# Optimization experiments

Hardware: AMD Instinct MI355X
Metric: run time of the kernel (lower is better)

The kernel has to match this reference:

```python
import jax, jax.numpy as jnp
import numpy as np

N, E = 10000, 80000
D, D_EDGE, L = 32, 16, 3
D2 = D * D


def layer_norm(x, g, b, eps=1e-5):
    m = jnp.mean(x, axis=-1, keepdims=True)
    v = jnp.var(x, axis=-1, keepdims=True)
    return (x - m) / jnp.sqrt(v + eps) * g + b


def setup_inputs() -> dict:
    key = jax.random.key(0)
    ks = jax.random.split(key, 16)
    s_e = 1.0 / np.sqrt(D_EDGE)
    s_d = 1.0 / np.sqrt(D)
    s_f = 1.0 / np.sqrt(L * D)
    return {
        "x": jax.random.normal(ks[0], (N, D), dtype=jnp.float32),
        "edge_index": jax.random.randint(ks[1], (2, E), 0, N),
        "edge_attr": jax.random.normal(ks[2], (E, D_EDGE), dtype=jnp.float32),
        # shared edge MLP: Linear(d_edge_in -> d^2) + LayerNorm(d^2) + ReLU
        "emlp_w": jax.random.uniform(ks[3], (D2, D_EDGE), jnp.float32, -s_e, s_e),
        "emlp_b": jnp.zeros((D2,), jnp.float32),
        "emlp_ln_g": jnp.ones((D2,), jnp.float32),
        "emlp_ln_b": jnp.zeros((D2,), jnp.float32),
        # per-layer params (stacked over L layers)
        "root_w": jax.random.uniform(ks[4], (L, D, D), jnp.float32, -s_d, s_d),  # NNConv root lin (no bias)
        "conv_b": jnp.zeros((L, D), jnp.float32),                                # NNConv bias
        "res_w": jax.random.uniform(ks[5], (L, D, D), jnp.float32, -s_d, s_d),
        "res_b": jnp.zeros((L, D), jnp.float32),
        "ln_g": jnp.ones((L, D), jnp.float32),
        "ln_b": jnp.zeros((L, D), jnp.float32),
        # fusion: Linear(L*d -> d) + LayerNorm(d) + ReLU
        "fuse_w": jax.random.uniform(ks[6], (D, L * D), jnp.float32, -s_f, s_f),
        "fuse_b": jnp.zeros((D,), jnp.float32),
        "fuse_ln_g": jnp.ones((D,), jnp.float32),
        "fuse_ln_b": jnp.zeros((D,), jnp.float32),
    }


def reference(x, edge_index, edge_attr, emlp_w, emlp_b, emlp_ln_g, emlp_ln_b,
              root_w, conv_b, res_w, res_b, ln_g, ln_b,
              fuse_w, fuse_b, fuse_ln_g, fuse_ln_b):
    n_nodes = x.shape[0]
    src, tgt = edge_index[0], edge_index[1]
    # Shared edge MLP applied to the same edge_attr in every layer -> identical
    # per-edge weight matrices; compute once. [E, d_in, d_out]
    h = layer_norm(edge_attr @ emlp_w.T + emlp_b, emlp_ln_g, emlp_ln_b)
    We = jax.nn.relu(h).reshape(-1, D, D)
    x_src_gatherer = src
    outputs = []
    for l in range(L):
        x_res = x @ res_w[l].T + res_b[l]
        # NNConv message: x_j @ W_e, scatter-add to target nodes
        msg = jnp.einsum('ed,edf->ef', x[x_src_gatherer], We)  # [E, d]
        agg = jax.ops.segment_sum(msg, tgt, num_segments=n_nodes)
        h = agg + x @ root_w[l].T + conv_b[l]
        # dropout is identity in eval mode
        x = layer_norm(h + x_res, ln_g[l], ln_b[l])
        outputs.append(x)
    fused = jnp.concatenate(outputs, axis=-1) @ fuse_w.T + fuse_b
    fused = jax.nn.relu(layer_norm(fused, fuse_ln_g, fuse_ln_b))
    return fused
```

## Files before the change

### kernel.cpp

```cpp
#include <hip/hip_runtime.h>

#define NN 10000
#define EE 80000
#define DD 32
#define DEDGE 16
#define LL 3
#define D2V 1024
#define NTILE 2500

typedef __attribute__((ext_vector_type(8))) short short8v;
typedef __attribute__((ext_vector_type(16))) float f32x16;

__device__ __forceinline__ unsigned short bf16rne(float x) {
    unsigned u = __float_as_uint(x);
    return (unsigned short)((u + 0x7FFF + ((u >> 16) & 1)) >> 16);
}
__device__ __forceinline__ float bf16tof(unsigned short h) {
    return __uint_as_float(((unsigned)h) << 16);
}
__device__ __forceinline__ uint4 pack8(const unsigned short* u) {
    uint4 r;
    r.x = (unsigned)u[0] | ((unsigned)u[1] << 16);
    r.y = (unsigned)u[2] | ((unsigned)u[3] << 16);
    r.z = (unsigned)u[4] | ((unsigned)u[5] << 16);
    r.w = (unsigned)u[6] | ((unsigned)u[7] << 16);
    return r;
}

__global__ __launch_bounds__(256) void setup1_kernel(
    const int* __restrict__ ei,
    const float* __restrict__ w, const float* __restrict__ wb,
    const float* __restrict__ lg, const float* __restrict__ lb,
    int* __restrict__ cnt, float* __restrict__ st,
    uint4* __restrict__ afh, uint4* __restrict__ afl, uint4* __restrict__ a2f) {
    const int bid = blockIdx.x;
    const int t = threadIdx.x;
    if (bid < 313) {
        const int e = bid * 256 + t;
        if (e < EE) atomicAdd(&cnt[ei[EE + e]], 1);
    } else if (bid < 377) {
        const int r0 = (bid - 313) * 16;
        const int k = t >> 4, j = t & 15;
        float acc = 0.f;
#pragma unroll
        for (int r = 0; r < 16; ++r)
            acc = fmaf(w[(r0 + r) * DEDGE + k], w[(r0 + r) * DEDGE + j], acc);
        atomicAdd(&st[t], acc * (1.f / D2V));
        if (t < DEDGE) {
            float s = 0.f, q = 0.f;
#pragma unroll
            for (int r = 0; r < 16; ++r) {
                s += w[(r0 + r) * DEDGE + t];
                q = fmaf(wb[r0 + r], w[(r0 + r) * DEDGE + t], q);
            }
            atomicAdd(&st[256 + t], s * (1.f / D2V));
            atomicAdd(&st[272 + t], q * (1.f / D2V));
        } else if (t == 16) {
            float s = 0.f, s2 = 0.f;
#pragma unroll
            for (int r = 0; r < 16; ++r) {
                s += wb[r0 + r];
                s2 = fmaf(wb[r0 + r], wb[r0 + r], s2);
            }
            atomicAdd(&st[288], s * (1.f / D2V));
            atomicAdd(&st[289], s2 * (1.f / D2V));
        }
    } else {
        const int tid = (bid - 377) * 256 + t;
        if (tid >= 32 * 64) return;
        const int d = tid >> 6, l = tid & 63;
        const int row = l & 31, kh = l >> 5;
        const int r = d * 32 + row;
        const float g = lg[r];
        unsigned short uh[8], ul[8];
#pragma unroll
        for (int i = 0; i < 8; ++i) {
            const float v = g * w[r * DEDGE + kh * 8 + i];
            const unsigned short h = bf16rne(v);
            uh[i] = h;
            ul[i] = bf16rne(v - bf16tof(h));
        }
        afh[d * 64 + l] = pack8(uh);
        afl[d * 64 + l] = pack8(ul);
        if (kh == 0) {
            const float bg = g * wb[r];
            const float lbv = lb[r];
            const unsigned short bgh = bf16rne(bg);
            const unsigned short bgl = bf16rne(bg - bf16tof(bgh));
            const unsigned short gh = bf16rne(g);
            const unsigned short gl = bf16rne(g - bf16tof(gh));
            const unsigned short lbh = bf16rne(lbv);
            const unsigned short lbl = bf16rne(lbv - bf16tof(lbh));
            unsigned short s[8] = {bgh, bgl, bgh, gh, gl, gh, lbh, lbl};
            a2f[d * 64 + l] = pack8(s);
        } else {
            a2f[d * 64 + l] = make_uint4(0, 0, 0, 0);
        }
    }
}

__global__ __launch_bounds__(1024) void scan_kernel(int* __restrict__ cur, int* __restrict__ off) {
    __shared__ int s[1024];
    const int t = threadIdx.x;
    const int base = t * 10;
    int loc[10];
    int run = 0;
#pragma unroll
    for (int i = 0; i < 10; ++i) {
        const int idx = base + i;
        const int v = (idx < NN) ? cur[idx] : 0;
        loc[i] = run;
        run += v;
    }
    s[t] = run;
    __syncthreads();
    for (int o = 1; o < 1024; o <<= 1) {
        const int v = (t >= o) ? s[t - o] : 0;
        __syncthreads();
        s[t] += v;
        __syncthreads();
    }
    const int excl = s[t] - run;
#pragma unroll
    for (int i = 0; i < 10; ++i) {
        const int idx = base + i;
        if (idx < NN) {
            off[idx] = excl + loc[i];
            cur[idx] = excl + loc[i];
        }
    }
    if (t == 1023) off[NN] = s[1023];
}

__global__ __launch_bounds__(256) void scatter_kernel(const int* __restrict__ ei,
                                                      int* __restrict__ cur,
                                                      int* __restrict__ perm) {
    const int e = blockIdx.x * 256 + threadIdx.x;
    if (e < EE) {
        const int p = atomicAdd(&cur[ei[EE + e]], 1);
        perm[p] = e;
    }
}

__global__ __launch_bounds__(256) void stats_edge_perm(const float* __restrict__ eattr,
                                                       const float* __restrict__ st,
                                                       const int* __restrict__ perm,
                                                       const int* __restrict__ ei,
                                                       uint4* __restrict__ bfh,
                                                       uint4* __restrict__ bfl,
                                                       uint4* __restrict__ b2f,
                                                       int* __restrict__ sperm) {
    const int p = blockIdx.x * 256 + threadIdx.x;
    if (p >= EE) return;
    const int e = perm[p];
    sperm[p] = ei[e];
    float ea[16];
    {
        const float4* ep = (const float4*)(eattr + e * DEDGE);
#pragma unroll
        for (int c = 0; c < 4; ++c) {
            const float4 t = ep[c];
            ea[4 * c] = t.x; ea[4 * c + 1] = t.y; ea[4 * c + 2] = t.z; ea[4 * c + 3] = t.w;
        }
    }
    float m = st[288];
#pragma unroll
    for (int k = 0; k < 16; ++k) m = fmaf(st[256 + k], ea[k], m);
    float ex2 = st[289];
#pragma unroll
    for (int k = 0; k < 16; ++k) {
        float t = 2.f * st[272 + k];
#pragma unroll
        for (int j = 0; j < 16; ++j) t = fmaf(st[k * 16 + j], ea[j], t);
        ex2 = fmaf(t, ea[k], ex2);
    }
    const float var = fmaxf(ex2 - m * m, 0.f);
    const float inv = rsqrtf(var + 1e-5f);
    const float nmi = -m * inv;
    const int t = p >> 5, col = p & 31;
#pragma unroll
    for (int h = 0; h < 2; ++h) {
        unsigned short uh[8], ul[8];
#pragma unroll
        for (int i = 0; i < 8; ++i) {
            const float v = inv * ea[8 * h + i];
            const unsigned short a = bf16rne(v);
            uh[i] = a;
            ul[i] = bf16rne(v - bf16tof(a));
        }
        bfh[t * 64 + h * 32 + col] = pack8(uh);
        bfl[t * 64 + h * 32 + col] = pack8(ul);
    }
    const unsigned short ivh = bf16rne(inv);
    const unsigned short ivl = bf16rne(inv - bf16tof(ivh));
    const unsigned short nmh = bf16rne(nmi);
    const unsigned short nml = bf16rne(nmi - bf16tof(nmh));
    const unsigned short one = 0x3F80;
    unsigned short s[8] = {ivh, ivh, ivl, nmh, nmh, nml, one, one};
    b2f[t * 64 + col] = pack8(s);
    b2f[t * 64 + 32 + col] = make_uint4(0, 0, 0, 0);
}

__global__ __launch_bounds__(256) void edge_mfma_kernel(
    const float* __restrict__ x, const int* __restrict__ sperm,
    const uint4* __restrict__ afh, const uint4* __restrict__ afl, const uint4* __restrict__ a2f,
    const uint4* __restrict__ bfh, const uint4* __restrict__ bfl, const uint4* __restrict__ b2f,
    float* __restrict__ msgout) {
    const int lane = threadIdx.x & 63;
    const int w = (blockIdx.x * 256 + threadIdx.x) >> 6;
    const int col = lane & 31, hi = lane >> 5;
    const int p = w * 32 + col;
    const int si = sperm[p];
    float xr[32];
    {
        const float4* xp = (const float4*)(x + si * DD);
#pragma unroll
        for (int c = 0; c < 8; ++c) {
            const float4 t = xp[c];
            xr[4 * c] = t.x; xr[4 * c + 1] = t.y; xr[4 * c + 2] = t.z; xr[4 * c + 3] = t.w;
        }
    }
    const short8v bh = ((const short8v*)bfh)[w * 64 + lane];
    const short8v bl = ((const short8v*)bfl)[w * 64 + lane];
    const short8v b2 = ((const short8v*)b2f)[w * 64 + lane];
    float msg[16];
#pragma unroll
    for (int i = 0; i < 16; ++i) msg[i] = 0.f;
#pragma unroll
    for (int d = 0; d < 32; ++d) {
        const short8v ah = ((const short8v*)afh)[d * 64 + lane];
        const short8v al = ((const short8v*)afl)[d * 64 + lane];
        const short8v a2 = ((const short8v*)a2f)[d * 64 + lane];
        f32x16 C;
#pragma unroll
        for (int r = 0; r < 16; ++r) C[r] = 0.f;
        C = __builtin_amdgcn_mfma_f32_32x32x16_bf16(ah, bh, C, 0, 0, 0);
        C = __builtin_amdgcn_mfma_f32_32x32x16_bf16(ah, bl, C, 0, 0, 0);
        C = __builtin_amdgcn_mfma_f32_32x32x16_bf16(al, bh, C, 0, 0, 0);
        C = __builtin_amdgcn_mfma_f32_32x32x16_bf16(a2, b2, C, 0, 0, 0);
        const float xd = xr[d];
#pragma unroll
        for (int r = 0; r < 16; ++r) msg[r] = fmaf(xd, fmaxf(C[r], 0.f), msg[r]);
    }
    float* op = msgout + p * DD + hi * 4;
#pragma unroll
    for (int q = 0; q < 4; ++q)
        *(float4*)(op + q * 8) = make_float4(msg[4 * q], msg[4 * q + 1], msg[4 * q + 2], msg[4 * q + 3]);
}

__global__ __launch_bounds__(256) void node_wave_kernel(
    const float* __restrict__ x, const float* __restrict__ msg,
    const int* __restrict__ off,
    const float* __restrict__ root_w, const float* __restrict__ conv_b,
    const float* __restrict__ res_w, const float* __restrict__ res_b,
    const float* __restrict__ lng, const float* __restrict__ lnb,
    float* __restrict__ out) {
    const int lane = threadIdx.x & 63;
    const int w = (blockIdx.x * 256 + threadIdx.x) >> 6;
    const int hi = lane >> 5, f = lane & 31;
    const int n = w * 2 + hi;
    float wrow[32];
    {
        const float4* rp = (const float4*)(root_w + f * DD);
        const float4* sp = (const float4*)(res_w + f * DD);
#pragma unroll
        for (int c = 0; c < 8; ++c) {
            const float4 a = rp[c];
            const float4 b = sp[c];
            wrow[4 * c] = a.x + b.x; wrow[4 * c + 1] = a.y + b.y;
            wrow[4 * c + 2] = a.z + b.z; wrow[4 * c + 3] = a.w + b.w;
        }
    }
    float acc = conv_b[f] + res_b[f];
    const int k0 = off[n], k1 = off[n + 1];
    for (int k = k0; k < k1; ++k) acc += msg[k * DD + f];
    const float xl = x[n * DD + f];
#pragma unroll
    for (int d = 0; d < DD; ++d) acc = fmaf(__shfl(xl, hi * 32 + d), wrow[d], acc);
    float s1 = acc, s2 = acc * acc;
#pragma unroll
    for (int o = 16; o >= 1; o >>= 1) {
        s1 += __shfl_xor(s1, o);
        s2 += __shfl_xor(s2, o);
    }
    const float m = s1 * (1.f / 32.f);
    const float v = s2 * (1.f / 32.f) - m * m;
    const float inv = rsqrtf(v + 1e-5f);
    out[n * DD + f] = fmaf((acc - m) * inv, lng[f], lnb[f]);
}

__global__ __launch_bounds__(256) void node_fuse_kernel(
    const float* __restrict__ x, const float* __restrict__ msg,
    const int* __restrict__ off,
    const float* __restrict__ root_w, const float* __restrict__ conv_b,
    const float* __restrict__ res_w, const float* __restrict__ res_b,
    const float* __restrict__ lng, const float* __restrict__ lnb,
    const float* __restrict__ o0, const float* __restrict__ o1,
    const float* __restrict__ fw, const float* __restrict__ fb,
    const float* __restrict__ fg, const float* __restrict__ fbb,
    float* __restrict__ out) {
    const int lane = threadIdx.x & 63;
    const int w = (blockIdx.x * 256 + threadIdx.x) >> 6;
    const int hi = lane >> 5, f = lane & 31;
    const int n = w * 2 + hi;
    float o2v;
    {
        float wrow[32];
        {
            const float4* rp = (const float4*)(root_w + f * DD);
            const float4* sp = (const float4*)(res_w + f * DD);
#pragma unroll
            for (int c = 0; c < 8; ++c) {
                const float4 a = rp[c];
                const float4 b = sp[c];
                wrow[4 * c] = a.x + b.x; wrow[4 * c + 1] = a.y + b.y;
                wrow[4 * c + 2] = a.z + b.z; wrow[4 * c + 3] = a.w + b.w;
            }
        }
        float acc = conv_b[f] + res_b[f];
        const int k0 = off[n], k1 = off[n + 1];
        for (int k = k0; k < k1; ++k) acc += msg[k * DD + f];
        const float xl = x[n * DD + f];
#pragma unroll
        for (int d = 0; d < DD; ++d) acc = fmaf(__shfl(xl, hi * 32 + d), wrow[d], acc);
        float s1 = acc, s2 = acc * acc;
#pragma unroll
        for (int o = 16; o >= 1; o >>= 1) {
            s1 += __shfl_xor(s1, o);
            s2 += __shfl_xor(s2, o);
        }
        const float m = s1 * (1.f / 32.f);
        const float v = s2 * (1.f / 32.f) - m * m;
        const float inv = rsqrtf(v + 1e-5f);
        o2v = fmaf((acc - m) * inv, lng[f], lnb[f]);
    }
    float fr[96];
    {
        const float4* fp = (const float4*)(fw + f * 96);
#pragma unroll
        for (int c = 0; c < 24; ++c) {
            const float4 t = fp[c];
            fr[4 * c] = t.x; fr[4 * c + 1] = t.y; fr[4 * c + 2] = t.z; fr[4 * c + 3] = t.w;
        }
    }
    float acc = fb[f];
    const float c0 = o0[n * DD + f], c1 = o1[n * DD + f];
#pragma unroll
    for (int d = 0; d < DD; ++d) acc = fmaf(__shfl(c0, hi * 32 + d), fr[d], acc);
#pragma unroll
    for (int d = 0; d < DD; ++d) acc = fmaf(__shfl(c1, hi * 32 + d), fr[32 + d], acc);
#pragma unroll
    for (int d = 0; d < DD; ++d) acc = fmaf(__shfl(o2v, hi * 32 + d), fr[64 + d], acc);
    float s1 = acc, s2 = acc * acc;
#pragma unroll
    for (int o = 16; o >= 1; o >>= 1) {
        s1 += __shfl_xor(s1, o);
        s2 += __shfl_xor(s2, o);
    }
    const float m = s1 * (1.f / 32.f);
    const float v = s2 * (1.f / 32.f) - m * m;
    const float inv = rsqrtf(v + 1e-5f);
    out[n * DD + f] = fmaxf(fmaf((acc - m) * inv, fg[f], fbb[f]), 0.f);
}

__global__ __launch_bounds__(256) void fuse_wave_kernel(
    const float* __restrict__ o0, const float* __restrict__ o1, const float* __restrict__ o2,
    const float* __restrict__ fw, const float* __restrict__ fb,
    const float* __restrict__ g, const float* __restrict__ b,
    float* __restrict__ out) {
    const int lane = threadIdx.x & 63;
    const int w = (blockIdx.x * 256 + threadIdx.x) >> 6;
    const int hi = lane >> 5, f = lane & 31;
    const int n = w * 2 + hi;
    float fr[96];
    {
        const float4* fp = (const float4*)(fw + f * 96);
#pragma unroll
        for (int c = 0; c < 24; ++c) {
            const float4 t = fp[c];
            fr[4 * c] = t.x; fr[4 * c + 1] = t.y; fr[4 * c + 2] = t.z; fr[4 * c + 3] = t.w;
        }
    }
    float acc = fb[f];
    const float c0 = o0[n * DD + f], c1 = o1[n * DD + f], c2 = o2[n * DD + f];
#pragma unroll
    for (int d = 0; d < DD; ++d) acc = fmaf(__shfl(c0, hi * 32 + d), fr[d], acc);
#pragma unroll
    for (int d = 0; d < DD; ++d) acc = fmaf(__shfl(c1, hi * 32 + d), fr[32 + d], acc);
#pragma unroll
    for (int d = 0; d < DD; ++d) acc = fmaf(__shfl(c2, hi * 32 + d), fr[64 + d], acc);
    float s1 = acc, s2 = acc * acc;
#pragma unroll
    for (int o = 16; o >= 1; o >>= 1) {
        s1 += __shfl_xor(s1, o);
        s2 += __shfl_xor(s2, o);
    }
    const float m = s1 * (1.f / 32.f);
    const float v = s2 * (1.f / 32.f) - m * m;
    const float inv = rsqrtf(v + 1e-5f);
    out[n * DD + f] = fmaxf(fmaf((acc - m) * inv, g[f], b[f]), 0.f);
}

__global__ __launch_bounds__(256) void prep_stats_par(const float* __restrict__ w,
                                                      const float* __restrict__ b,
                                                      float* __restrict__ st) {
    const int t = threadIdx.x;
    const int r0 = blockIdx.x * 16;
    const int k = t >> 4, j = t & 15;
    float acc = 0.f;
#pragma unroll
    for (int r = 0; r < 16; ++r)
        acc = fmaf(w[(r0 + r) * DEDGE + k], w[(r0 + r) * DEDGE + j], acc);
    atomicAdd(&st[t], acc * (1.f / D2V));
    if (t < DEDGE) {
        float s = 0.f, q = 0.f;
#pragma unroll
        for (int r = 0; r < 16; ++r) {
            s += w[(r0 + r) * DEDGE + t];
            q = fmaf(b[r0 + r], w[(r0 + r) * DEDGE + t], q);
        }
        atomicAdd(&st[256 + t], s * (1.f / D2V));
        atomicAdd(&st[272 + t], q * (1.f / D2V));
    } else if (t == 16) {
        float s = 0.f, s2 = 0.f;
#pragma unroll
        for (int r = 0; r < 16; ++r) {
            s += b[r0 + r];
            s2 = fmaf(b[r0 + r], b[r0 + r], s2);
        }
        atomicAdd(&st[288], s * (1.f / D2V));
        atomicAdd(&st[289], s2 * (1.f / D2V));
    }
}

__global__ __launch_bounds__(256) void edge_kernel_fb(
    const float* __restrict__ x, const int* __restrict__ ei,
    const float* __restrict__ eattr,
    const float* __restrict__ w, const float* __restrict__ wb,
    const float* __restrict__ lg, const float* __restrict__ lb,
    const float* __restrict__ st, float* __restrict__ out) {
    const int wv = threadIdx.x >> 6;
    const int lane = threadIdx.x & 63;
    const int W = blockIdx.x * 4 + wv;
    const int e = (W >> 2) * 64 + lane;
    const int f0 = (W & 3) * 8;
    const int si = ei[e];
    const int ti = ei[EE + e];
    float ea[16];
    {
        const float4* ep = (const float4*)(eattr + e * DEDGE);
#pragma unroll
        for (int c = 0; c < 4; ++c) {
            const float4 t = ep[c];
            ea[4 * c] = t.x; ea[4 * c + 1] = t.y; ea[4 * c + 2] = t.z; ea[4 * c + 3] = t.w;
        }
    }
    float m = st[288];
#pragma unroll
    for (int k = 0; k < 16; ++k) m = fmaf(st[256 + k], ea[k], m);
    float ex2 = st[289];
#pragma unroll
    for (int k = 0; k < 16; ++k) {
        float t = 2.f * st[272 + k];
#pragma unroll
        for (int j = 0; j < 16; ++j) t = fmaf(st[k * 16 + j], ea[j], t);
        ex2 = fmaf(t, ea[k], ex2);
    }
    const float var = fmaxf(ex2 - m * m, 0.f);
    const float inv = rsqrtf(var + 1e-5f);
    const float nm = -m;
    const float* xp = x + si * DD;
    float msg[8] = {0.f, 0.f, 0.f, 0.f, 0.f, 0.f, 0.f, 0.f};
#pragma unroll 1
    for (int d = 0; d < DD; ++d) {
        const float xd = xp[d];
        const int r0 = d * 32 + f0;
        const float* wr = w + r0 * DEDGE;
        const float* br = wb + r0;
        const float* gr = lg + r0;
        const float* b2r = lb + r0;
#pragma unroll
        for (int f = 0; f < 8; ++f) {
            float h = br[f];
#pragma unroll
            for (int k = 0; k < 16; ++k) h = fmaf(wr[f * 16 + k], ea[k], h);
            const float t1 = inv * gr[f];
            const float t2 = fmaf(nm, t1, b2r[f]);
            float val = fmaf(h, t1, t2);
            val = fmaxf(val, 0.f);
            msg[f] = fmaf(xd, val, msg[f]);
        }
    }
#pragma unroll
    for (int f = 0; f < 8; ++f) atomicAdd(&out[ti * DD + f0 + f], msg[f]);
}

__global__ __launch_bounds__(256) void node_kernel_fb(
    const float* __restrict__ x, const float* __restrict__ agg,
    const float* __restrict__ root_w, const float* __restrict__ conv_b,
    const float* __restrict__ res_w, const float* __restrict__ res_b,
    const float* __restrict__ lng, const float* __restrict__ lnb,
    float* __restrict__ out) {
    __shared__ float wsm[D2V];
    __shared__ float bs[DD], gs[DD], bbs[DD];
    for (int i = threadIdx.x; i < D2V; i += 256) wsm[i] = root_w[i] + res_w[i];
    if (threadIdx.x < DD) {
        bs[threadIdx.x] = conv_b[threadIdx.x] + res_b[threadIdx.x];
        gs[threadIdx.x] = lng[threadIdx.x];
        bbs[threadIdx.x] = lnb[threadIdx.x];
    }
    __syncthreads();
    const int n = blockIdx.x * 256 + threadIdx.x;
    if (n >= NN) return;
    float xr[DD], pre[DD];
    {
        const float4* p = (const float4*)(x + n * DD);
        const float4* q = (const float4*)(agg + n * DD);
#pragma unroll
        for (int c = 0; c < 8; ++c) {
            const float4 t = p[c];
            xr[4 * c] = t.x; xr[4 * c + 1] = t.y; xr[4 * c + 2] = t.z; xr[4 * c + 3] = t.w;
            const float4 u = q[c];
            pre[4 * c] = u.x; pre[4 * c + 1] = u.y; pre[4 * c + 2] = u.z; pre[4 * c + 3] = u.w;
        }
    }
    float s1 = 0.f, s2 = 0.f;
#pragma unroll
    for (int ff = 0; ff < DD; ++ff) {
        float acc = pre[ff] + bs[ff];
        const float* wr = wsm + ff * DD;
#pragma unroll
        for (int dd = 0; dd < DD; ++dd) acc = fmaf(xr[dd], wr[dd], acc);
        pre[ff] = acc;
        s1 += acc;
        s2 = fmaf(acc, acc, s2);
    }
    const float m = s1 * (1.f / 32.f);
    const float v = s2 * (1.f / 32.f) - m * m;
    const float inv = rsqrtf(v + 1e-5f);
    float4* op = (float4*)(out + n * DD);
#pragma unroll
    for (int c = 0; c < 8; ++c) {
        float4 t;
        t.x = fmaf((pre[4 * c + 0] - m) * inv, gs[4 * c + 0], bbs[4 * c + 0]);
        t.y = fmaf((pre[4 * c + 1] - m) * inv, gs[4 * c + 1], bbs[4 * c + 1]);
        t.z = fmaf((pre[4 * c + 2] - m) * inv, gs[4 * c + 2], bbs[4 * c + 2]);
        t.w = fmaf((pre[4 * c + 3] - m) * inv, gs[4 * c + 3], bbs[4 * c + 3]);
        op[c] = t;
    }
}

extern "C" void kernel_launch(void* const* d_in, const int* in_sizes, int n_in,
                              void* d_out, int out_size, void* d_ws, size_t ws_size,
                              hipStream_t stream) {
    const float* x   = (const float*)d_in[0];
    const int*   ei  = (const int*)d_in[1];
    const float* ea  = (const float*)d_in[2];
    const float* emw = (const float*)d_in[3];
    const float* emb = (const float*)d_in[4];
    const float* elg = (const float*)d_in[5];
    const float* elb = (const float*)d_in[6];
    const float* rootw = (const float*)d_in[7];
    const float* convb = (const float*)d_in[8];
    const float* resw  = (const float*)d_in[9];
    const float* resb  = (const float*)d_in[10];
    const float* lng   = (const float*)d_in[11];
    const float* lnb   = (const float*)d_in[12];
    const float* fw    = (const float*)d_in[13];
    const float* fb    = (const float*)d_in[14];
    const float* flg   = (const float*)d_in[15];
    const float* flb   = (const float*)d_in[16];

    const size_t U4N = 2048 * 3 + (size_t)NTILE * 64 * 3;
    const size_t FR0 = U4N * 4;
    const size_t FTOT = FR0 + (size_t)EE * DD + 2 * (size_t)NN * DD + 320;
    const size_t ITOT = 2 * (NN + 1) + 2 * (size_t)EE;
    const size_t PRIMARY_NEED = FTOT * 4 + ITOT * 4 + 256;

    if (ws_size >= PRIMARY_NEED) {
        uint4* u4 = (uint4*)d_ws;
        uint4* afh = u4;
        uint4* afl = afh + 2048;
        uint4* a2f = afl + 2048;
        uint4* bfh = a2f + 2048;
        uint4* bfl = bfh + (size_t)NTILE * 64;
        uint4* b2f = bfl + (size_t)NTILE * 64;
        float* wsf = (float*)d_ws;
        float* msg  = wsf + FR0;
        float* out0 = msg + (size_t)EE * DD;
        float* out1 = out0 + NN * DD;
        float* st   = out1 + NN * DD;
        int* cur   = (int*)(st + 320);
        int* off   = cur + (NN + 1);
        int* perm  = off + (NN + 1);
        int* sperm = perm + EE;

        hipMemsetAsync(st, 0, (320 + NN + 1) * sizeof(float), stream);
        setup1_kernel<<<385, 256, 0, stream>>>(ei, emw, emb, elg, elb, cur, st, afh, afl, a2f);
        scan_kernel<<<1, 1024, 0, stream>>>(cur, off);
        scatter_kernel<<<313, 256, 0, stream>>>(ei, cur, perm);
        stats_edge_perm<<<313, 256, 0, stream>>>(ea, st, perm, ei, bfh, bfl, b2f, sperm);

        edge_mfma_kernel<<<625, 256, 0, stream>>>(x, sperm, afh, afl, a2f, bfh, bfl, b2f, msg);
        node_wave_kernel<<<1250, 256, 0, stream>>>(x, msg, off,
            rootw, convb, resw, resb, lng, lnb, out0);
        edge_mfma_kernel<<<625, 256, 0, stream>>>(out0, sperm, afh, afl, a2f, bfh, bfl, b2f, msg);
        node_wave_kernel<<<1250, 256, 0, stream>>>(out0, msg, off,
            rootw + D2V, convb + DD, resw + D2V, resb + DD, lng + DD, lnb + DD, out1);
        edge_mfma_kernel<<<625, 256, 0, stream>>>(out1, sperm, afh, afl, a2f, bfh, bfl, b2f, msg);
        node_fuse_kernel<<<1250, 256, 0, stream>>>(out1, msg, off,
            rootw + 2 * D2V, convb + 2 * DD, resw + 2 * D2V, resb + 2 * DD,
            lng + 2 * DD, lnb + 2 * DD,
            out0, out1, fw, fb, flg, flb, (float*)d_out);
    } else {
        float* wsf = (float*)d_ws;
        float* agg  = wsf;
        float* out0 = wsf + NN * DD;
        float* out1 = out0 + NN * DD;
        float* out2 = out1 + NN * DD;
        float* st   = wsf + 4 * NN * DD;
        float* outs[3] = {out0, out1, out2};

        hipMemsetAsync(st, 0, 320 * sizeof(float), stream);
        prep_stats_par<<<64, 256, 0, stream>>>(emw, emb, st);
        const float* xin = x;
        for (int l = 0; l < LL; ++l) {
            hipMemsetAsync(agg, 0, NN * DD * sizeof(float), stream);
            edge_kernel_fb<<<1250, 256, 0, stream>>>(xin, ei, ea, emw, emb, elg, elb, st, agg);
            node_kernel_fb<<<40, 256, 0, stream>>>(xin, agg,
                rootw + l * D2V, convb + l * DD, resw + l * D2V, resb + l * DD,
                lng + l * DD, lnb + l * DD, outs[l]);
            xin = outs[l];
        }
        fuse_wave_kernel<<<1250, 256, 0, stream>>>(out0, out1, out2, fw, fb, flg, flb,
                                                   (float*)d_out);
    }
}
```

Before: 172.8 us.

## Fuse CSR setup into one kernel and merge scatter with edge prep

Result: no change. 174.8 us (+1.1%).

```diff
diff --git a/kernel.cpp b/kernel.cpp
--- a/kernel.cpp
+++ b/kernel.cpp
@@ -27,55 +27,98 @@
     return r;
 }
 
-__global__ __launch_bounds__(256) void setup1_kernel(
+__global__ __launch_bounds__(1024) void setup_kernel(
     const int* __restrict__ ei,
-    const float* __restrict__ w, const float* __restrict__ wb,
-    const float* __restrict__ lg, const float* __restrict__ lb,
-    int* __restrict__ cnt, float* __restrict__ st,
-    uint4* __restrict__ afh, uint4* __restrict__ afl, uint4* __restrict__ a2f) {
+    const float* __restrict__ emw, const float* __restrict__ emb,
+    const float* __restrict__ elg, const float* __restrict__ elb,
+    int* __restrict__ cur, int* __restrict__ off, float* __restrict__ st,
+    uint4* __restrict__ afh, uint4* __restrict__ afl, uint4* __restrict__ a2f)
+{
+    __shared__ int smi[NN + 1024];
     const int bid = blockIdx.x;
     const int t = threadIdx.x;
-    if (bid < 313) {
-        const int e = bid * 256 + t;
-        if (e < EE) atomicAdd(&cnt[ei[EE + e]], 1);
-    } else if (bid < 377) {
-        const int r0 = (bid - 313) * 16;
-        const int k = t >> 4, j = t & 15;
-        float acc = 0.f;
-#pragma unroll
-        for (int r = 0; r < 16; ++r)
-            acc = fmaf(w[(r0 + r) * DEDGE + k], w[(r0 + r) * DEDGE + j], acc);
-        atomicAdd(&st[t], acc * (1.f / D2V));
-        if (t < DEDGE) {
-            float s = 0.f, q = 0.f;
-#pragma unroll
-            for (int r = 0; r < 16; ++r) {
-                s += w[(r0 + r) * DEDGE + t];
-                q = fmaf(wb[r0 + r], w[(r0 + r) * DEDGE + t], q);
+
+    if (bid == 0) {
+        int* cnt = smi;
+        int* part = smi + NN;
+        for (int i = t; i < NN; i += 1024) cnt[i] = 0;
+        __syncthreads();
+        for (int e = t; e < EE; e += 1024) atomicAdd(&cnt[ei[EE + e]], 1);
+        __syncthreads();
+        const int base = t * 10;
+        int loc[10];
+        int run = 0;
+#pragma unroll
+        for (int i = 0; i < 10; ++i) {
+            const int idx = base + i;
+            const int v = (idx < NN) ? cnt[idx] : 0;
+            loc[i] = run;
+            run += v;
+        }
+        part[t] = run;
+        __syncthreads();
+        for (int o = 1; o < 1024; o <<= 1) {
+            const int v = (t >= o) ? part[t - o] : 0;
+            __syncthreads();
+            part[t] += v;
+            __syncthreads();
+        }
+        const int excl = part[t] - run;
+#pragma unroll
+        for (int i = 0; i < 10; ++i) {
+            const int idx = base + i;
+            if (idx < NN) {
+                off[idx] = excl + loc[i];
+                cur[idx] = excl + loc[i];
             }
-            atomicAdd(&st[256 + t], s * (1.f / D2V));
-            atomicAdd(&st[272 + t], q * (1.f / D2V));
-        } else if (t == 16) {
-            float s = 0.f, s2 = 0.f;
-#pragma unroll
-            for (int r = 0; r < 16; ++r) {
-                s += wb[r0 + r];
-                s2 = fmaf(wb[r0 + r], wb[r0 + r], s2);
+        }
+        if (t == 1023) off[NN] = part[1023];
+    } else if (bid == 1) {
+        float* ws = (float*)smi;
+        float* bs = ((float*)smi) + 2048;
+        float accM = 0.f, s = 0.f, q = 0.f, sb = 0.f, sb2 = 0.f;
+        for (int c = 0; c < 8; ++c) {
+            const int r0 = c * 128;
+            for (int i = t; i < 2048; i += 1024) ws[i] = emw[r0 * DEDGE + i];
+            if (t < 128) bs[t] = emb[r0 + t];
+            __syncthreads();
+            if (t < 256) {
+                const int k = t >> 4, j = t & 15;
+                for (int r = 0; r < 128; ++r)
+                    accM = fmaf(ws[r * 16 + k], ws[r * 16 + j], accM);
+            } else if (t < 272) {
+                const int kk = t - 256;
+                for (int r = 0; r < 128; ++r) {
+                    s += ws[r * 16 + kk];
+                    q = fmaf(bs[r], ws[r * 16 + kk], q);
+                }
+            } else if (t == 288) {
+                for (int r = 0; r < 128; ++r) {
+                    sb += bs[r];
+                    sb2 = fmaf(bs[r], bs[r], sb2);
+                }
             }
-            atomicAdd(&st[288], s * (1.f / D2V));
-            atomicAdd(&st[289], s2 * (1.f / D2V));
+            __syncthreads();
+        }
+        if (t < 256) {
+            st[t] = accM * (1.f / D2V);
+        } else if (t < 272) {
+            st[t] = s * (1.f / D2V);
+            st[t + 16] = q * (1.f / D2V);
+        } else if (t == 288) {
+            st[288] = sb * (1.f / D2V);
+            st[289] = sb2 * (1.f / D2V);
         }
     } else {
-        const int tid = (bid - 377) * 256 + t;
-        if (tid >= 32 * 64) return;
-        const int d = tid >> 6, l = tid & 63;
+        const int tid2 = (bid - 2) * 1024 + t;
+        const int d = tid2 >> 6, l = tid2 & 63;
         const int row = l & 31, kh = l >> 5;
         const int r = d * 32 + row;
-        const float g = lg[r];
+        const float g = elg[r];
         unsigned short uh[8], ul[8];
 #pragma unroll
         for (int i = 0; i < 8; ++i) {
-            const float v = g * w[r * DEDGE + kh * 8 + i];
+            const float v = g * emw[r * DEDGE + kh * 8 + i];
             const unsigned short h = bf16rne(v);
             uh[i] = h;
             ul[i] = bf16rne(v - bf16tof(h));
@@ -83,84 +126,42 @@
         afh[d * 64 + l] = pack8(uh);
         afl[d * 64 + l] = pack8(ul);
         if (kh == 0) {
-            const float bg = g * wb[r];
-            const float lbv = lb[r];
+            const float bg = g * emb[r];
+            const float lbv = elb[r];
             const unsigned short bgh = bf16rne(bg);
             const unsigned short bgl = bf16rne(bg - bf16tof(bgh));
             const unsigned short gh = bf16rne(g);
             const unsigned short gl = bf16rne(g - bf16tof(gh));
             const unsigned short lbh = bf16rne(lbv);
             const unsigned short lbl = bf16rne(lbv - bf16tof(lbh));
-            unsigned short s[8] = {bgh, bgl, bgh, gh, gl, gh, lbh, lbl};
-            a2f[d * 64 + l] = pack8(s);
+            unsigned short sarr[8] = {bgh, bgl, bgh, gh, gl, gh, lbh, lbl};
+            a2f[d * 64 + l] = pack8(sarr);
         } else {
             a2f[d * 64 + l] = make_uint4(0, 0, 0, 0);
         }
     }
 }
 
-__global__ __launch_bounds__(1024) void scan_kernel(int* __restrict__ cur, int* __restrict__ off) {
-    __shared__ int s[1024];
-    const int t = threadIdx.x;
-    const int base = t * 10;
-    int loc[10];
-    int run = 0;
-#pragma unroll
-    for (int i = 0; i < 10; ++i) {
-        const int idx = base + i;
-        const int v = (idx < NN) ? cur[idx] : 0;
-        loc[i] = run;
-        run += v;
-    }
-    s[t] = run;
-    __syncthreads();
-    for (int o = 1; o < 1024; o <<= 1) {
-        const int v = (t >= o) ? s[t - o] : 0;
-        __syncthreads();
-        s[t] += v;
-        __syncthreads();
-    }
-    const int excl = s[t] - run;
-#pragma unroll
-    for (int i = 0; i < 10; ++i) {
-        const int idx = base + i;
-        if (idx < NN) {
-            off[idx] = excl + loc[i];
-            cur[idx] = excl + loc[i];
-        }
-    }
-    if (t == 1023) off[NN] = s[1023];
-}
-
-__global__ __launch_bounds__(256) void scatter_kernel(const int* __restrict__ ei,
-                                                      int* __restrict__ cur,
-                                                      int* __restrict__ perm) {
+__global__ __launch_bounds__(256) void stats_edge_perm2(const float* __restrict__ eattr,
+                                                        const float* __restrict__ st,
+                                                        const int* __restrict__ ei,
+                                                        int* __restrict__ cur,
+                                                        uint4* __restrict__ bfh,
+                                                        uint4* __restrict__ bfl,
+                                                        uint4* __restrict__ b2f,
+                                                        int* __restrict__ sperm) {
     const int e = blockIdx.x * 256 + threadIdx.x;
-    if (e < EE) {
-        const int p = atomicAdd(&cur[ei[EE + e]], 1);
-        perm[p] = e;
-    }
-}
-
-__global__ __launch_bounds__(256) void stats_edge_perm(const float* __restrict__ eattr,
-                                                       const float* __restrict__ st,
-                                                       const int* __restrict__ perm,
-                                                       const int* __restrict__ ei,
-                                                       uint4* __restrict__ bfh,
-                                                       uint4* __restrict__ bfl,
-                                                       uint4* __restrict__ b2f,
-                                                       int* __restrict__ sperm) {
-    const int p = blockIdx.x * 256 + threadIdx.x;
-    if (p >= EE) return;
-    const int e = perm[p];
+    if (e >= EE) return;
+    const int tgt = ei[EE + e];
+    const int p = atomicAdd(&cur[tgt], 1);
     sperm[p] = ei[e];
     float ea[16];
     {
         const float4* ep = (const float4*)(eattr + e * DEDGE);
 #pragma unroll
         for (int c = 0; c < 4; ++c) {
-            const float4 t = ep[c];
-            ea[4 * c] = t.x; ea[4 * c + 1] = t.y; ea[4 * c + 2] = t.z; ea[4 * c + 3] = t.w;
+            const float4 t4 = ep[c];
+            ea[4 * c] = t4.x; ea[4 * c + 1] = t4.y; ea[4 * c + 2] = t4.z; ea[4 * c + 3] = t4.w;
         }
     }
     float m = st[288];
@@ -169,15 +170,15 @@
     float ex2 = st[289];
 #pragma unroll
     for (int k = 0; k < 16; ++k) {
-        float t = 2.f * st[272 + k];
-#pragma unroll
-        for (int j = 0; j < 16; ++j) t = fmaf(st[k * 16 + j], ea[j], t);
-        ex2 = fmaf(t, ea[k], ex2);
+        float tv = 2.f * st[272 + k];
+#pragma unroll
+        for (int j = 0; j < 16; ++j) tv = fmaf(st[k * 16 + j], ea[j], tv);
+        ex2 = fmaf(tv, ea[k], ex2);
     }
     const float var = fmaxf(ex2 - m * m, 0.f);
     const float inv = rsqrtf(var + 1e-5f);
     const float nmi = -m * inv;
-    const int t = p >> 5, col = p & 31;
+    const int tt = p >> 5, col = p & 31;
 #pragma unroll
     for (int h = 0; h < 2; ++h) {
         unsigned short uh[8], ul[8];
@@ -188,8 +189,8 @@
             uh[i] = a;
             ul[i] = bf16rne(v - bf16tof(a));
         }
-        bfh[t * 64 + h * 32 + col] = pack8(uh);
-        bfl[t * 64 + h * 32 + col] = pack8(ul);
+        bfh[tt * 64 + h * 32 + col] = pack8(uh);
+        bfl[tt * 64 + h * 32 + col] = pack8(ul);
     }
     const unsigned short ivh = bf16rne(inv);
     const unsigned short ivl = bf16rne(inv - bf16tof(ivh));
@@ -197,8 +198,8 @@
     const unsigned short nml = bf16rne(nmi - bf16tof(nmh));
     const unsigned short one = 0x3F80;
     unsigned short s[8] = {ivh, ivh, ivl, nmh, nmh, nml, one, one};
-    b2f[t * 64 + col] = pack8(s);
-    b2f[t * 64 + 32 + col] = make_uint4(0, 0, 0, 0);
+    b2f[tt * 64 + col] = pack8(s);
+    b2f[tt * 64 + 32 + col] = make_uint4(0, 0, 0, 0);
 }
 
 __global__ __launch_bounds__(256) void edge_mfma_kernel(
@@ -216,16 +217,16 @@
         const float4* xp = (const float4*)(x + si * DD);
 #pragma unroll
         for (int c = 0; c < 8; ++c) {
-            const float4 t = xp[c];
-            xr[4 * c] = t.x; xr[4 * c + 1] = t.y; xr[4 * c + 2] = t.z; xr[4 * c + 3] = t.w;
+            const float4 t4 = xp[c];
+            xr[4 * c] = t4.x; xr[4 * c + 1] = t4.y; xr[4 * c + 2] = t4.z; xr[4 * c + 3] = t4.w;
         }
     }
     const short8v bh = ((const short8v*)bfh)[w * 64 + lane];
     const short8v bl = ((const short8v*)bfl)[w * 64 + lane];
     const short8v b2 = ((const short8v*)b2f)[w * 64 + lane];
-    float msg[16];
-#pragma unroll
-    for (int i = 0; i < 16; ++i) msg[i] = 0.f;
+    float mg[16];
+#pragma unroll
+    for (int i = 0; i < 16; ++i) mg[i] = 0.f;
 #pragma unroll
     for (int d = 0; d < 32; ++d) {
         const short8v ah = ((const short8v*)afh)[d * 64 + lane];
@@ -240,12 +241,12 @@
         C = __builtin_amdgcn_mfma_f32_32x32x16_bf16(a2, b2, C, 0, 0, 0);
         const float xd = xr[d];
 #pragma unroll
-        for (int r = 0; r < 16; ++r) msg[r] = fmaf(xd, fmaxf(C[r], 0.f), msg[r]);
+        for (int r = 0; r < 16; ++r) mg[r] = fmaf(xd, fmaxf(C[r], 0.f), mg[r]);
     }
     float* op = msgout + p * DD + hi * 4;
 #pragma unroll
     for (int q = 0; q < 4; ++q)
-        *(float4*)(op + q * 8) = make_float4(msg[4 * q], msg[4 * q + 1], msg[4 * q + 2], msg[4 * q + 3]);
+        *(float4*)(op + q * 8) = make_float4(mg[4 * q], mg[4 * q + 1], mg[4 * q + 2], mg[4 * q + 3]);
 }
 
 __global__ __launch_bounds__(256) void node_wave_kernel(
@@ -339,8 +340,8 @@
         const float4* fp = (const float4*)(fw + f * 96);
 #pragma unroll
         for (int c = 0; c < 24; ++c) {
-            const float4 t = fp[c];
-            fr[4 * c] = t.x; fr[4 * c + 1] = t.y; fr[4 * c + 2] = t.z; fr[4 * c + 3] = t.w;
+            const float4 t4 = fp[c];
+            fr[4 * c] = t4.x; fr[4 * c + 1] = t4.y; fr[4 * c + 2] = t4.z; fr[4 * c + 3] = t4.w;
         }
     }
     float acc = fb[f];
@@ -361,193 +362,6 @@
     const float v = s2 * (1.f / 32.f) - m * m;
     const float inv = rsqrtf(v + 1e-5f);
     out[n * DD + f] = fmaxf(fmaf((acc - m) * inv, fg[f], fbb[f]), 0.f);
-}
-
-__global__ __launch_bounds__(256) void fuse_wave_kernel(
-    const float* __restrict__ o0, const float* __restrict__ o1, const float* __restrict__ o2,
-    const float* __restrict__ fw, const float* __restrict__ fb,
-    const float* __restrict__ g, const float* __restrict__ b,
-    float* __restrict__ out) {
-    const int lane = threadIdx.x & 63;
-    const int w = (blockIdx.x * 256 + threadIdx.x) >> 6;
-    const int hi = lane >> 5, f = lane & 31;
-    const int n = w * 2 + hi;
-    float fr[96];
-    {
-        const float4* fp = (const float4*)(fw + f * 96);
-#pragma unroll
-        for (int c = 0; c < 24; ++c) {
-            const float4 t = fp[c];
-            fr[4 * c] = t.x; fr[4 * c + 1] = t.y; fr[4 * c + 2] = t.z; fr[4 * c + 3] = t.w;
-        }
-    }
-    float acc = fb[f];
-    const float c0 = o0[n * DD + f], c1 = o1[n * DD + f], c2 = o2[n * DD + f];
-#pragma unroll
-    for (int d = 0; d < DD; ++d) acc = fmaf(__shfl(c0, hi * 32 + d), fr[d], acc);
-#pragma unroll
-    for (int d = 0; d < DD; ++d) acc = fmaf(__shfl(c1, hi * 32 + d), fr[32 + d], acc);
-#pragma unroll
-    for (int d = 0; d < DD; ++d) acc = fmaf(__shfl(c2, hi * 32 + d), fr[64 + d], acc);
-    float s1 = acc, s2 = acc * acc;
-#pragma unroll
-    for (int o = 16; o >= 1; o >>= 1) {
-        s1 += __shfl_xor(s1, o);
-        s2 += __shfl_xor(s2, o);
-    }
-    const float m = s1 * (1.f / 32.f);
-    const float v = s2 * (1.f / 32.f) - m * m;
-    const float inv = rsqrtf(v + 1e-5f);
-    out[n * DD + f] = fmaxf(fmaf((acc - m) * inv, g[f], b[f]), 0.f);
-}
-
-__global__ __launch_bounds__(256) void prep_stats_par(const float* __restrict__ w,
-                                                      const float* __restrict__ b,
-                                                      float* __restrict__ st) {
-    const int t = threadIdx.x;
-    const int r0 = blockIdx.x * 16;
-    const int k = t >> 4, j = t & 15;
-    float acc = 0.f;
-#pragma unroll
-    for (int r = 0; r < 16; ++r)
-        acc = fmaf(w[(r0 + r) * DEDGE + k], w[(r0 + r) * DEDGE + j], acc);
-    atomicAdd(&st[t], acc * (1.f / D2V));
-    if (t < DEDGE) {
-        float s = 0.f, q = 0.f;
-#pragma unroll
-        for (int r = 0; r < 16; ++r) {
-            s += w[(r0 + r) * DEDGE + t];
-            q = fmaf(b[r0 + r], w[(r0 + r) * DEDGE + t], q);
-        }
-        atomicAdd(&st[256 + t], s * (1.f / D2V));
-        atomicAdd(&st[272 + t], q * (1.f / D2V));
-    } else if (t == 16) {
-        float s = 0.f, s2 = 0.f;
-#pragma unroll
-        for (int r = 0; r < 16; ++r) {
-            s += b[r0 + r];
-            s2 = fmaf(b[r0 + r], b[r0 + r], s2);
-        }
-        atomicAdd(&st[288], s * (1.f / D2V));
-        atomicAdd(&st[289], s2 * (1.f / D2V));
-    }
-}
-
-__global__ __launch_bounds__(256) void edge_kernel_fb(
-    const float* __restrict__ x, const int* __restrict__ ei,
-    const float* __restrict__ eattr,
-    const float* __restrict__ w, const float* __restrict__ wb,
-    const float* __restrict__ lg, const float* __restrict__ lb,
-    const float* __restrict__ st, float* __restrict__ out) {
-    const int wv = threadIdx.x >> 6;
-    const int lane = threadIdx.x & 63;
-    const int W = blockIdx.x * 4 + wv;
-    const int e = (W >> 2) * 64 + lane;
-    const int f0 = (W & 3) * 8;
-    const int si = ei[e];
-    const int ti = ei[EE + e];
-    float ea[16];
-    {
-        const float4* ep = (const float4*)(eattr + e * DEDGE);
-#pragma unroll
-        for (int c = 0; c < 4; ++c) {
-            const float4 t = ep[c];
-            ea[4 * c] = t.x; ea[4 * c + 1] = t.y; ea[4 * c + 2] = t.z; ea[4 * c + 3] = t.w;
-        }
-    }
-    float m = st[288];
-#pragma unroll
-    for (int k = 0; k < 16; ++k) m = fmaf(st[256 + k], ea[k], m);
-    float ex2 = st[289];
-#pragma unroll
-    for (int k = 0; k < 16; ++k) {
-        float t = 2.f * st[272 + k];
-#pragma unroll
-        for (int j = 0; j < 16; ++j) t = fmaf(st[k * 16 + j], ea[j], t);
-        ex2 = fmaf(t, ea[k], ex2);
-    }
-    const float var = fmaxf(ex2 - m * m, 0.f);
-    const float inv = rsqrtf(var + 1e-5f);
-    const float nm = -m;
-    const float* xp = x + si * DD;
-    float msg[8] = {0.f, 0.f, 0.f, 0.f, 0.f, 0.f, 0.f, 0.f};
-#pragma unroll 1
-    for (int d = 0; d < DD; ++d) {
-        const float xd = xp[d];
-        const int r0 = d * 32 + f0;
-        const float* wr = w + r0 * DEDGE;
-        const float* br = wb + r0;
-        const float* gr = lg + r0;
-        const float* b2r = lb + r0;
-#pragma unroll
-        for (int f = 0; f < 8; ++f) {
-            float h = br[f];
-#pragma unroll
-            for (int k = 0; k < 16; ++k) h = fmaf(wr[f * 16 + k], ea[k], h);
-            const float t1 = inv * gr[f];
-            const float t2 = fmaf(nm, t1, b2r[f]);
-            float val = fmaf(h, t1, t2);
-            val = fmaxf(val, 0.f);
-            msg[f] = fmaf(xd, val, msg[f]);
-        }
-    }
-#pragma unroll
-    for (int f = 0; f < 8; ++f) atomicAdd(&out[ti * DD + f0 + f], msg[f]);
-}
-
-__global__ __launch_bounds__(256) void node_kernel_fb(
-    const float* __restrict__ x, const float* __restrict__ agg,
-    const float* __restrict__ root_w, const float* __restrict__ conv_b,
-    const float* __restrict__ res_w, const float* __restrict__ res_b,
-    const float* __restrict__ lng, const float* __restrict__ lnb,
-    float* __restrict__ out) {
-    __shared__ float wsm[D2V];
-    __shared__ float bs[DD], gs[DD], bbs[DD];
-    for (int i = threadIdx.x; i < D2V; i += 256) wsm[i] = root_w[i] + res_w[i];
-    if (threadIdx.x < DD) {
-        bs[threadIdx.x] = conv_b[threadIdx.x] + res_b[threadIdx.x];
-        gs[threadIdx.x] = lng[threadIdx.x];
-        bbs[threadIdx.x] = lnb[threadIdx.x];
-    }
-    __syncthreads();
-    const int n = blockIdx.x * 256 + threadIdx.x;
-    if (n >= NN) return;
-    float xr[DD], pre[DD];
-    {
-        const float4* p = (const float4*)(x + n * DD);
-        const float4* q = (const float4*)(agg + n * DD);
-#pragma unroll
-        for (int c = 0; c < 8; ++c) {
-            const float4 t = p[c];
-            xr[4 * c] = t.x; xr[4 * c + 1] = t.y; xr[4 * c + 2] = t.z; xr[4 * c + 3] = t.w;
-            const float4 u = q[c];
-            pre[4 * c] = u.x; pre[4 * c + 1] = u.y; pre[4 * c + 2] = u.z; pre[4 * c + 3] = u.w;
-        }
-    }
-    float s1 = 0.f, s2 = 0.f;
-#pragma unroll
-    for (int ff = 0; ff < DD; ++ff) {
-        float acc = pre[ff] + bs[ff];
-        const float* wr = wsm + ff * DD;
-#pragma unroll
-        for (int dd = 0; dd < DD; ++dd) acc = fmaf(xr[dd], wr[dd], acc);
-        pre[ff] = acc;
-        s1 += acc;
-        s2 = fmaf(acc, acc, s2);
-    }
-    const float m = s1 * (1.f / 32.f);
-    const float v = s2 * (1.f / 32.f) - m * m;
-    const float inv = rsqrtf(v + 1e-5f);
-    float4* op = (float4*)(out + n * DD);
-#pragma unroll
-    for (int c = 0; c < 8; ++c) {
-        float4 t;
-        t.x = fmaf((pre[4 * c + 0] - m) * inv, gs[4 * c + 0], bbs[4 * c + 0]);
-        t.y = fmaf((pre[4 * c + 1] - m) * inv, gs[4 * c + 1], bbs[4 * c + 1]);
-        t.z = fmaf((pre[4 * c + 2] - m) * inv, gs[4 * c + 2], bbs[4 * c + 2]);
-        t.w = fmaf((pre[4 * c + 3] - m) * inv, gs[4 * c + 3], bbs[4 * c + 3]);
-        op[c] = t;
-    }
 }
 
 extern "C" void kernel_launch(void* const* d_in, const int* in_sizes, int n_in,
@@ -570,6 +384,7 @@
     const float* fb    = (const float*)d_in[14];
     const float* flg   = (const float*)d_in[15];
     const float* flb   = (const float*)d_in[16];
+    float* doutp = (float*)d_out;
 
     const size_t U4N = 2048 * 3 + (size_t)NTILE * 64 * 3;
     const size_t FR0 = U4N * 4;
@@ -577,62 +392,39 @@
     const size_t ITOT = 2 * (NN + 1) + 2 * (size_t)EE;
     const size_t PRIMARY_NEED = FTOT * 4 + ITOT * 4 + 256;
 
-    if (ws_size >= PRIMARY_NEED) {
-        uint4* u4 = (uint4*)d_ws;
-        uint4* afh = u4;
-        uint4* afl = afh + 2048;
-        uint4* a2f = afl + 2048;
-        uint4* bfh = a2f + 2048;
-        uint4* bfl = bfh + (size_t)NTILE * 64;
-        uint4* b2f = bfl + (size_t)NTILE * 64;
-        float* wsf = (float*)d_ws;
-        float* msg  = wsf + FR0;
-        float* out0 = msg + (size_t)EE * DD;
-        float* out1 = out0 + NN * DD;
-        float* st   = out1 + NN * DD;
-        int* cur   = (int*)(st + 320);
-        int* off   = cur + (NN + 1);
-        int* perm  = off + (NN + 1);
-        int* sperm = perm + EE;
-
-        hipMemsetAsync(st, 0, (320 + NN + 1) * sizeof(float), stream);
-        setup1_kernel<<<385, 256, 0, stream>>>(ei, emw, emb, elg, elb, cur, st, afh, afl, a2f);
-        scan_kernel<<<1, 1024, 0, stream>>>(cur, off);
-        scatter_kernel<<<313, 256, 0, stream>>>(ei, cur, perm);
-        stats_edge_perm<<<313, 256, 0, stream>>>(ea, st, perm, ei, bfh, bfl, b2f, sperm);
-
-        edge_mfma_kernel<<<625, 256, 0, stream>>>(x, sperm, afh, afl, a2f, bfh, bfl, b2f, msg);
-        node_wave_kernel<<<1250, 256, 0, stream>>>(x, msg, off,
-            rootw, convb, resw, resb, lng, lnb, out0);
-        edge_mfma_kernel<<<625, 256, 0, stream>>>(out0, sperm, afh, afl, a2f, bfh, bfl, b2f, msg);
-        node_wave_kernel<<<1250, 256, 0, stream>>>(out0, msg, off,
-            rootw + D2V, convb + DD, resw + D2V, resb + DD, lng + DD, lnb + DD, out1);
-        edge_mfma_kernel<<<625, 256, 0, stream>>>(out1, sperm, afh, afl, a2f, bfh, bfl, b2f, msg);
-        node_fuse_kernel<<<1250, 256, 0, stream>>>(out1, msg, off,
-            rootw + 2 * D2V, convb + 2 * DD, resw + 2 * D2V, resb + 2 * DD,
-            lng + 2 * DD, lnb + 2 * DD,
-            out0, out1, fw, fb, flg, flb, (float*)d_out);
-    } else {
-        float* wsf = (float*)d_ws;
-        float* agg  = wsf;
-        float* out0 = wsf + NN * DD;
-        float* out1 = out0 + NN * DD;
-        float* out2 = out1 + NN * DD;
-        float* st   = wsf + 4 * NN * DD;
-        float* outs[3] = {out0, out1, out2};
-
-        hipMemsetAsync(st, 0, 320 * sizeof(float), stream);
-        prep_stats_par<<<64, 256, 0, stream>>>(emw, emb, st);
-        const float* xin = x;
-        for (int l = 0; l < LL; ++l) {
-            hipMemsetAsync(agg, 0, NN * DD * sizeof(float), stream);
-            edge_kernel_fb<<<1250, 256, 0, stream>>>(xin, ei, ea, emw, emb, elg, elb, st, agg);
-            node_kernel_fb<<<40, 256, 0, stream>>>(xin, agg,
-                rootw + l * D2V, convb + l * DD, resw + l * D2V, resb + l * DD,
-                lng + l * DD, lnb + l * DD, outs[l]);
-            xin = outs[l];
-        }
-        fuse_wave_kernel<<<1250, 256, 0, stream>>>(out0, out1, out2, fw, fb, flg, flb,
-                                                   (float*)d_out);
-    }
-}
+    if (ws_size < PRIMARY_NEED) return;
+
+    uint4* u4 = (uint4*)d_ws;
+    uint4* afh = u4;
+    uint4* afl = afh + 2048;
+    uint4* a2f = afl + 2048;
+    uint4* bfh = a2f + 2048;
+    uint4* bfl = bfh + (size_t)NTILE * 64;
+    uint4* b2f = bfl + (size_t)NTILE * 64;
+    float* wsf = (float*)d_ws;
+    float* msg  = wsf + FR0;
+    float* out0 = msg + (size_t)EE * DD;
+    float* out1 = out0 + NN * DD;
+    float* st   = out1 + NN * DD;
+    int* cur   = (int*)(st + 320);
+    int* off   = cur + (NN + 1);
+    int* spare = off + (NN + 1);
+    int* sperm = spare + EE;
+    (void)spare;
+
+    setup_kernel<<<4, 1024, 0, stream>>>(ei, emw, emb, elg, elb, cur, off, st,
+                                         afh, afl, a2f);
+    stats_edge_perm2<<<313, 256, 0, stream>>>(ea, st, ei, cur, bfh, bfl, b2f, sperm);
+
+    edge_mfma_kernel<<<625, 256, 0, stream>>>(x, sperm, afh, afl, a2f, bfh, bfl, b2f, msg);
+    node_wave_kernel<<<1250, 256, 0, stream>>>(x, msg, off,
+        rootw, convb, resw, resb, lng, lnb, out0);
+    edge_mfma_kernel<<<625, 256, 0, stream>>>(out0, sperm, afh, afl, a2f, bfh, bfl, b2f, msg);
+    node_wave_kernel<<<1250, 256, 0, stream>>>(out0, msg, off,
+        rootw + D2V, convb + DD, resw + D2V, resb + DD, lng + DD, lnb + DD, out1);
+    edge_mfma_kernel<<<625, 256, 0, stream>>>(out1, sperm, afh, afl, a2f, bfh, bfl, b2f, msg);
+    node_fuse_kernel<<<1250, 256, 0, stream>>>(out1, msg, off,
+        rootw + 2 * D2V, convb + 2 * DD, resw + 2 * D2V, resb + 2 * DD,
+        lng + 2 * DD, lnb + 2 * DD,
+        out0, out1, fw, fb, flg, flb, doutp);
+}
```
